# Kernel tuning notes

Hardware: AMD Instinct MI355X
Metric: run time of the kernel (lower is better)

Reference implementation:

```python
import jax, jax.numpy as jnp
import numpy as np

FH, FW, CIN, COUT = 5, 5, 3, 16
PATCH = FH * FW * CIN  # 75
ALPHA = 1.0


def smooth_max(xk, axis):
    # alpha-softmax smooth maximum: sum(x * exp(alpha*x)) / sum(exp(alpha*x))
    w = jax.nn.softmax(ALPHA * xk, axis=axis)
    return jnp.sum(w * xk, axis=axis)


def setup_inputs() -> dict:
    key = jax.random.key(0)
    k_x, k_k1, k_k2 = jax.random.split(key, 3)
    B, Hout, Wout = 2, 220, 220
    x = jax.random.normal(k_x, (B, PATCH, Hout, Wout), dtype=jnp.float32)
    # xavier_uniform for kernel shape (fh, fw, cin, cout): fan_in=fh*fw*cin? torch treats
    # dims [..0]=fan stuff; a small uniform init is faithful enough for a numeric baseline.
    lim = float(np.sqrt(6.0 / (PATCH + COUT)))
    k1 = jax.random.uniform(k_k1, (FH, FW, CIN, COUT), jnp.float32, -lim, lim)
    k2 = jax.random.uniform(k_k2, (FH, FW, CIN, COUT), jnp.float32, -lim, lim)
    bias = jnp.zeros((COUT,), dtype=jnp.float32)
    return {"x": x, "k1": k1, "k2": k2, "bias": bias}


def reference(x, k1, k2, bias):
    # x: (B, patch_dim, Hout, Wout) unfolded patches
    k1f = k1.reshape(PATCH, COUT)  # (patch_dim, out_ch)
    k2f = k2.reshape(PATCH, COUT)
    # broadcast add: (B, patch_dim, out_ch, H, W)
    xk1 = x[:, :, None, :, :] + k1f[None, :, :, None, None]
    y11 = smooth_max(xk1, axis=1)  # (B, out_ch, H, W)
    xk2 = (-x)[:, :, None, :, :] + k2f[None, :, :, None, None]
    y22 = smooth_max(xk2, axis=1)
    return y11 + y22 + bias[None, :, None, None]
```

## Files before the change

### kernel.cpp

```cpp
#include <hip/hip_runtime.h>

#define HWD    48400
#define PATCHD 75
#define NPOS   96800
#define LOG2E  1.44269504088896340736f

typedef __attribute__((ext_vector_type(8))) _Float16 f16x8;
typedef __attribute__((ext_vector_type(2))) __fp16   h16x2;
typedef __attribute__((ext_vector_type(4))) float    f32x4;

union U2 { h16x2 h; unsigned u; };
union UF { unsigned u[4]; f16x8 v; };

__global__ void smorph_build_tables(const float* __restrict__ k1,
                                    const float* __restrict__ k2,
                                    _Float16* __restrict__ tbl)
{
    int i = (int)blockIdx.x * 256 + (int)threadIdx.x;
    if (i >= 4 * 3 * 4 * 16 * 8) return;
    const int j = i & 7;
    const int c = (i >> 3) & 15;
    const int g = (i >> 7) & 3;
    const int t = i >> 9;
    const int s = t % 3;
    const int r = t / 3;
    const int k = 32 * s + 8 * g + j;
    float val = 0.f;
    if (k < PATCHD) {
        const float* kw = (r < 2) ? k1 : k2;
        const float w = kw[k * 16 + c];
        const float e = __expf(w);
        val = (r & 1) ? (w * e) : e;
    }
    tbl[i] = (_Float16)val;
}

__global__ __launch_bounds__(256, 3)
void smorph_mfma8(const float* __restrict__ x,
                  const _Float16* __restrict__ tbl,
                  const float* __restrict__ bias,
                  float* __restrict__ out)
{
    const int tid = (int)threadIdx.x;
    const int l   = tid & 63;
    const int w   = tid >> 6;
    const int g   = l >> 4;
    const int c   = l & 15;

    int bb = (int)blockIdx.x * 128;
    if (bb > NPOS - 128) bb = NPOS - 128;
    const int pA = bb + w * 32;
    const int pB = pA + 16;
    const int bA = (pA >= HWD) ? 1 : 0;
    const int bB = (pB >= HWD) ? 1 : 0;
    const int hwA = pA - bA * HWD;
    const int hwB = pB - bB * HWD;
    const float* xbA = x + (size_t)bA * PATCHD * HWD + hwA + c;
    const float* xbB = x + (size_t)bB * PATCHD * HWD + hwB + c;

    const f16x8* tf = (const f16x8*)tbl;
    const int fbase = g * 16 + c;
    f16x8 Tf[12];
    #pragma unroll
    for (int t = 0; t < 12; ++t) Tf[t] = tf[t * 64 + fbase];

    float xvA[24], xvB[24];
    #pragma unroll
    for (int s = 0; s < 3; ++s)
        #pragma unroll
        for (int j = 0; j < 8; ++j) {
            int k = 32 * s + 8 * g + j;
            k = (k > PATCHD - 1) ? (PATCHD - 1) : k;
            xvA[s * 8 + j] = xbA[(size_t)k * HWD];
            xvB[s * 8 + j] = xbB[(size_t)k * HWD];
        }

    f32x4 aN1A = {0.f,0.f,0.f,0.f}, aD1A = {0.f,0.f,0.f,0.f};
    f32x4 aN2A = {0.f,0.f,0.f,0.f}, aD2A = {0.f,0.f,0.f,0.f};
    f32x4 aN1B = {0.f,0.f,0.f,0.f}, aD1B = {0.f,0.f,0.f,0.f};
    f32x4 aN2B = {0.f,0.f,0.f,0.f}, aD2B = {0.f,0.f,0.f,0.f};

    #define COMP(src, aN1, aD1, aN2, aD2)                                     \
        _Pragma("unroll")                                                     \
        for (int s = 0; s < 3; ++s) {                                         \
            float E[8], R[8];                                                 \
            _Pragma("unroll")                                                 \
            for (int j = 0; j < 8; ++j) {                                     \
                const float t_ = (src)[s * 8 + j] * LOG2E;                    \
                E[j] = __builtin_amdgcn_exp2f(t_);                            \
                R[j] = __builtin_amdgcn_exp2f(-t_);                           \
            }                                                                 \
            UF fEx, fE, fRx, fR;                                              \
            _Pragma("unroll")                                                 \
            for (int jp = 0; jp < 4; ++jp) {                                  \
                const float x0 = (src)[s * 8 + 2 * jp];                       \
                const float x1 = (src)[s * 8 + 2 * jp + 1];                   \
                U2 q;                                                         \
                q.h = __builtin_amdgcn_cvt_pkrtz(E[2*jp] * x0,  E[2*jp+1] * x1);  fEx.u[jp] = q.u; \
                q.h = __builtin_amdgcn_cvt_pkrtz(E[2*jp],       E[2*jp+1]);       fE.u[jp]  = q.u; \
                q.h = __builtin_amdgcn_cvt_pkrtz(-R[2*jp] * x0, -R[2*jp+1] * x1); fRx.u[jp] = q.u; \
                q.h = __builtin_amdgcn_cvt_pkrtz(R[2*jp],       R[2*jp+1]);       fR.u[jp]  = q.u; \
            }                                                                 \
            aN1 = __builtin_amdgcn_mfma_f32_16x16x32_f16(Tf[0 + s], fEx.v, aN1, 0, 0, 0); \
            aN1 = __builtin_amdgcn_mfma_f32_16x16x32_f16(Tf[3 + s], fE.v,  aN1, 0, 0, 0); \
            aD1 = __builtin_amdgcn_mfma_f32_16x16x32_f16(Tf[0 + s], fE.v,  aD1, 0, 0, 0); \
            aN2 = __builtin_amdgcn_mfma_f32_16x16x32_f16(Tf[6 + s], fRx.v, aN2, 0, 0, 0); \
            aN2 = __builtin_amdgcn_mfma_f32_16x16x32_f16(Tf[9 + s], fR.v,  aN2, 0, 0, 0); \
            aD2 = __builtin_amdgcn_mfma_f32_16x16x32_f16(Tf[6 + s], fR.v,  aD2, 0, 0, 0); \
        }

    COMP(xvA, aN1A, aD1A, aN2A, aD2A)
    COMP(xvB, aN1B, aD1B, aN2B, aD2B)
    #undef COMP

    const float4 bsv = *(const float4*)(bias + 4 * g);
    float* obA = out + ((size_t)(bA * 16 + 4 * g)) * HWD + hwA + c;
    float* obB = out + ((size_t)(bB * 16 + 4 * g)) * HWD + hwB + c;
    #pragma unroll
    for (int r = 0; r < 4; ++r) {
        const float bsr = (r == 0) ? bsv.x : (r == 1) ? bsv.y : (r == 2) ? bsv.z : bsv.w;
        obA[(size_t)r * HWD] = aN1A[r] * __builtin_amdgcn_rcpf(aD1A[r])
                             + aN2A[r] * __builtin_amdgcn_rcpf(aD2A[r]) + bsr;
        obB[(size_t)r * HWD] = aN1B[r] * __builtin_amdgcn_rcpf(aD1B[r])
                             + aN2B[r] * __builtin_amdgcn_rcpf(aD2B[r]) + bsr;
    }
}

extern "C" void kernel_launch(void* const* d_in, const int* in_sizes, int n_in,
                              void* d_out, int out_size, void* d_ws, size_t ws_size,
                              hipStream_t stream)
{
    const float* x    = (const float*)d_in[0];
    const float* k1   = (const float*)d_in[1];
    const float* k2   = (const float*)d_in[2];
    const float* bias = (const float*)d_in[3];
    float* out = (float*)d_out;
    _Float16* tbl = (_Float16*)d_ws;

    smorph_build_tables<<<(4 * 3 * 4 * 16 * 8 + 255) / 256, 256, 0, stream>>>(k1, k2, tbl);
    smorph_mfma8<<<(NPOS + 127) / 128, 256, 0, stream>>>(x, tbl, bias, out);
}
```

Baseline: 17.51 us.

## Stage inputs through LDS with async global-to-LDS loads and double buffering

```diff
diff --git a/kernel.cpp b/kernel.cpp
--- a/kernel.cpp
+++ b/kernel.cpp
@@ -3,6 +3,7 @@
 #define HWD    48400
 #define PATCHD 75
 #define NPOS   96800
+#define XBAT   3630000
 #define LOG2E  1.44269504088896340736f
 
 typedef __attribute__((ext_vector_type(8))) _Float16 f16x8;
@@ -11,6 +12,10 @@
 
 union U2 { h16x2 h; unsigned u; };
 union UF { unsigned u[4]; f16x8 v; };
+
+#define GLOAD_LDS16(gp, lp) __builtin_amdgcn_global_load_lds(             \
+    (const __attribute__((address_space(1))) void*)(gp),                  \
+    (__attribute__((address_space(3))) void*)(lp), 16, 0, 0)
 
 __global__ void smorph_build_tables(const float* __restrict__ k1,
                                     const float* __restrict__ k2,
@@ -36,27 +41,21 @@
 }
 
 __global__ __launch_bounds__(256, 3)
-void smorph_mfma8(const float* __restrict__ x,
+void smorph_mfma9(const float* __restrict__ x,
                   const _Float16* __restrict__ tbl,
                   const float* __restrict__ bias,
                   float* __restrict__ out)
 {
+    __shared__ __align__(16) float sX[2][32][128];
+
     const int tid = (int)threadIdx.x;
     const int l   = tid & 63;
     const int w   = tid >> 6;
     const int g   = l >> 4;
     const int c   = l & 15;
 
-    int bb = (int)blockIdx.x * 128;
-    if (bb > NPOS - 128) bb = NPOS - 128;
-    const int pA = bb + w * 32;
-    const int pB = pA + 16;
-    const int bA = (pA >= HWD) ? 1 : 0;
-    const int bB = (pB >= HWD) ? 1 : 0;
-    const int hwA = pA - bA * HWD;
-    const int hwB = pB - bB * HWD;
-    const float* xbA = x + (size_t)bA * PATCHD * HWD + hwA + c;
-    const float* xbB = x + (size_t)bB * PATCHD * HWD + hwB + c;
+    int pbase = (int)blockIdx.x * 128;
+    if (pbase > NPOS - 128) pbase = NPOS - 128;
 
     const f16x8* tf = (const f16x8*)tbl;
     const int fbase = g * 16 + c;
@@ -64,15 +63,21 @@
     #pragma unroll
     for (int t = 0; t < 12; ++t) Tf[t] = tf[t * 64 + fbase];
 
-    float xvA[24], xvB[24];
-    #pragma unroll
-    for (int s = 0; s < 3; ++s)
-        #pragma unroll
-        for (int j = 0; j < 8; ++j) {
-            int k = 32 * s + 8 * g + j;
-            k = (k > PATCHD - 1) ? (PATCHD - 1) : k;
-            xvA[s * 8 + j] = xbA[(size_t)k * HWD];
-            xvB[s * 8 + j] = xbB[(size_t)k * HWD];
+    const int lhi = l >> 5;
+    const int llo = l & 31;
+    const int ps  = pbase + 4 * llo;
+    const int sb  = (ps >= HWD) ? 1 : 0;
+    const float* sgb = x + (size_t)sb * XBAT + (ps - sb * HWD);
+
+    #define STAGE(buf, s)                                                     \
+        {                                                                     \
+            _Pragma("unroll")                                                 \
+            for (int i_ = 0; i_ < 4; ++i_) {                                  \
+                const int kg_ = 32 * (s) + w * 8 + 2 * i_ + lhi;              \
+                if (kg_ < PATCHD)                                             \
+                    GLOAD_LDS16(sgb + (size_t)kg_ * HWD,                      \
+                                &sX[buf][w * 8 + 2 * i_][0]);                 \
+            }                                                                 \
         }
 
     f32x4 aN1A = {0.f,0.f,0.f,0.f}, aD1A = {0.f,0.f,0.f,0.f};
@@ -80,49 +85,77 @@
     f32x4 aN1B = {0.f,0.f,0.f,0.f}, aD1B = {0.f,0.f,0.f,0.f};
     f32x4 aN2B = {0.f,0.f,0.f,0.f}, aD2B = {0.f,0.f,0.f,0.f};
 
-    #define COMP(src, aN1, aD1, aN2, aD2)                                     \
-        _Pragma("unroll")                                                     \
-        for (int s = 0; s < 3; ++s) {                                         \
+    #define COMP(buf, s, T, aN1, aD1, aN2, aD2)                               \
+        {                                                                     \
+            float xv[8];                                                      \
+            _Pragma("unroll")                                                 \
+            for (int j_ = 0; j_ < 8; ++j_) {                                  \
+                float v_ = sX[buf][8 * g + j_][w * 32 + (T) * 16 + c];        \
+                if ((s) == 2 && (8 * g + j_ >= PATCHD - 64)) v_ = 0.f;        \
+                xv[j_] = v_;                                                  \
+            }                                                                 \
             float E[8], R[8];                                                 \
             _Pragma("unroll")                                                 \
-            for (int j = 0; j < 8; ++j) {                                     \
-                const float t_ = (src)[s * 8 + j] * LOG2E;                    \
-                E[j] = __builtin_amdgcn_exp2f(t_);                            \
-                R[j] = __builtin_amdgcn_exp2f(-t_);                           \
+            for (int j_ = 0; j_ < 8; ++j_) {                                  \
+                const float t_ = xv[j_] * LOG2E;                              \
+                E[j_] = __builtin_amdgcn_exp2f(t_);                           \
+                R[j_] = __builtin_amdgcn_exp2f(-t_);                          \
             }                                                                 \
             UF fEx, fE, fRx, fR;                                              \
             _Pragma("unroll")                                                 \
             for (int jp = 0; jp < 4; ++jp) {                                  \
-                const float x0 = (src)[s * 8 + 2 * jp];                       \
-                const float x1 = (src)[s * 8 + 2 * jp + 1];                   \
+                const float x0 = xv[2*jp], x1 = xv[2*jp+1];                   \
                 U2 q;                                                         \
                 q.h = __builtin_amdgcn_cvt_pkrtz(E[2*jp] * x0,  E[2*jp+1] * x1);  fEx.u[jp] = q.u; \
                 q.h = __builtin_amdgcn_cvt_pkrtz(E[2*jp],       E[2*jp+1]);       fE.u[jp]  = q.u; \
                 q.h = __builtin_amdgcn_cvt_pkrtz(-R[2*jp] * x0, -R[2*jp+1] * x1); fRx.u[jp] = q.u; \
                 q.h = __builtin_amdgcn_cvt_pkrtz(R[2*jp],       R[2*jp+1]);       fR.u[jp]  = q.u; \
             }                                                                 \
-            aN1 = __builtin_amdgcn_mfma_f32_16x16x32_f16(Tf[0 + s], fEx.v, aN1, 0, 0, 0); \
-            aN1 = __builtin_amdgcn_mfma_f32_16x16x32_f16(Tf[3 + s], fE.v,  aN1, 0, 0, 0); \
-            aD1 = __builtin_amdgcn_mfma_f32_16x16x32_f16(Tf[0 + s], fE.v,  aD1, 0, 0, 0); \
-            aN2 = __builtin_amdgcn_mfma_f32_16x16x32_f16(Tf[6 + s], fRx.v, aN2, 0, 0, 0); \
-            aN2 = __builtin_amdgcn_mfma_f32_16x16x32_f16(Tf[9 + s], fR.v,  aN2, 0, 0, 0); \
-            aD2 = __builtin_amdgcn_mfma_f32_16x16x32_f16(Tf[6 + s], fR.v,  aD2, 0, 0, 0); \
+            aN1 = __builtin_amdgcn_mfma_f32_16x16x32_f16(Tf[0 + (s)], fEx.v, aN1, 0, 0, 0); \
+            aN1 = __builtin_amdgcn_mfma_f32_16x16x32_f16(Tf[3 + (s)], fE.v,  aN1, 0, 0, 0); \
+            aD1 = __builtin_amdgcn_mfma_f32_16x16x32_f16(Tf[0 + (s)], fE.v,  aD1, 0, 0, 0); \
+            aN2 = __builtin_amdgcn_mfma_f32_16x16x32_f16(Tf[6 + (s)], fRx.v, aN2, 0, 0, 0); \
+            aN2 = __builtin_amdgcn_mfma_f32_16x16x32_f16(Tf[9 + (s)], fR.v,  aN2, 0, 0, 0); \
+            aD2 = __builtin_amdgcn_mfma_f32_16x16x32_f16(Tf[6 + (s)], fR.v,  aD2, 0, 0, 0); \
         }
 
-    COMP(xvA, aN1A, aD1A, aN2A, aD2A)
-    COMP(xvB, aN1B, aD1B, aN2B, aD2B)
+    STAGE(0, 0);
+    __syncthreads();
+    STAGE(1, 1);
+    COMP(0, 0, 0, aN1A, aD1A, aN2A, aD2A);
+    COMP(0, 0, 1, aN1B, aD1B, aN2B, aD2B);
+    __syncthreads();
+    STAGE(0, 2);
+    COMP(1, 1, 0, aN1A, aD1A, aN2A, aD2A);
+    COMP(1, 1, 1, aN1B, aD1B, aN2B, aD2B);
+    __syncthreads();
+    COMP(0, 2, 0, aN1A, aD1A, aN2A, aD2A);
+    COMP(0, 2, 1, aN1B, aD1B, aN2B, aD2B);
+    #undef STAGE
     #undef COMP
 
     const float4 bsv = *(const float4*)(bias + 4 * g);
-    float* obA = out + ((size_t)(bA * 16 + 4 * g)) * HWD + hwA + c;
-    float* obB = out + ((size_t)(bB * 16 + 4 * g)) * HWD + hwB + c;
+    float (*sY)[128] = (float (*)[128])&sX[1][0][0];
     #pragma unroll
     for (int r = 0; r < 4; ++r) {
         const float bsr = (r == 0) ? bsv.x : (r == 1) ? bsv.y : (r == 2) ? bsv.z : bsv.w;
-        obA[(size_t)r * HWD] = aN1A[r] * __builtin_amdgcn_rcpf(aD1A[r])
-                             + aN2A[r] * __builtin_amdgcn_rcpf(aD2A[r]) + bsr;
-        obB[(size_t)r * HWD] = aN1B[r] * __builtin_amdgcn_rcpf(aD1B[r])
-                             + aN2B[r] * __builtin_amdgcn_rcpf(aD2B[r]) + bsr;
+        const float yA = aN1A[r] * __builtin_amdgcn_rcpf(aD1A[r])
+                       + aN2A[r] * __builtin_amdgcn_rcpf(aD2A[r]) + bsr;
+        const float yB = aN1B[r] * __builtin_amdgcn_rcpf(aD1B[r])
+                       + aN2B[r] * __builtin_amdgcn_rcpf(aD2B[r]) + bsr;
+        sY[4 * g + r][w * 32 + 0 * 16 + c] = yA;
+        sY[4 * g + r][w * 32 + 1 * 16 + c] = yB;
+    }
+    __syncthreads();
+
+    #pragma unroll
+    for (int p = 0; p < 2; ++p) {
+        const int ch = p * 8 + (tid >> 5);
+        const int l5 = tid & 31;
+        const int pp = pbase + 4 * l5;
+        const int ob = (pp >= HWD) ? 1 : 0;
+        const float4 vv = *(const float4*)&sY[ch][4 * l5];
+        *(float4*)(out + ((size_t)(ob * 16 + ch)) * HWD + (pp - ob * HWD)) = vv;
     }
 }
 
@@ -138,5 +171,5 @@
     _Float16* tbl = (_Float16*)d_ws;
 
     smorph_build_tables<<<(4 * 3 * 4 * 16 * 8 + 255) / 256, 256, 0, stream>>>(k1, k2, tbl);
-    smorph_mfma8<<<(NPOS + 127) / 128, 256, 0, stream>>>(x, tbl, bias, out);
+    smorph_mfma9<<<(NPOS + 127) / 128, 256, 0, stream>>>(x, tbl, bias, out);
 }
```

Measured after the change: 17.72 us. Within noise of the previous version (+1.2%).
